# Optimization experiments

Hardware: AMD Instinct MI355X
Metric: run time of the kernel (lower is better)

## Reference

```python
import jax, jax.numpy as jnp
import numpy as np

B, C, H, W = 16, 128, 64, 64
LN_EPS = 1e-5


def _gru_dir(x, w_ih, w_hh, b_ih, b_hh, reverse):
    # x: [N, T, C]; PyTorch GRU cell math:
    # r = sig(Wir x + bir + Whr h + bhr); z = sig(Wiz x + biz + Whz h + bhz)
    xp = jnp.einsum('ntc,gc->ntg', x, w_ih) + b_ih  # [N,T,3C] precomputed input gates
    xs = jnp.swapaxes(xp, 0, 1)  # [T,N,3C]
    h0 = jnp.zeros((x.shape[0], w_hh.shape[1]), x.dtype)

    def step(h, xt):
        g = h @ w_hh.T + b_hh
        xr, xz, xn = jnp.split(xt, 3, axis=-1)
        hr, hz, hn = jnp.split(g, 3, axis=-1)
        r = jax.nn.sigmoid(xr + hr)
        z = jax.nn.sigmoid(xz + hz)
        n = jnp.tanh(xn + r * hn)
        h2 = (1.0 - z) * n + z * h
        return h2, h2

    _, ys = jax.lax.scan(step, h0, xs, reverse=reverse)
    return jnp.swapaxes(ys, 0, 1)  # [N,T,C]


def _gru_bidir(x, wih_f, whh_f, bih_f, bhh_f, wih_b, whh_b, bib_b, bhh_b):
    of = _gru_dir(x, wih_f, whh_f, bih_f, bhh_f, False)
    ob = _gru_dir(x, wih_b, whh_b, bib_b, bhh_b, True)
    return jnp.concatenate([of, ob], axis=-1)  # [N,T,2C]


def _forward(x, ln_g, ln_b,
             h_wih_f, h_whh_f, h_bih_f, h_bhh_f,
             h_wih_b, h_whh_b, h_bih_b, h_bhh_b,
             w_wih_f, w_whh_f, w_bih_f, w_bhh_f,
             w_wih_b, w_whh_b, w_bih_b, w_bhh_b,
             proj_w, proj_b):
    Bn, Cc, Hh, Ww = x.shape
    x_flat = x.reshape(Bn, Cc, Hh * Ww).transpose(0, 2, 1)  # b (h w) c
    mu = x_flat.mean(-1, keepdims=True)
    var = ((x_flat - mu) ** 2).mean(-1, keepdims=True)
    xn = (x_flat - mu) * jax.lax.rsqrt(var + LN_EPS) * ln_g + ln_b
    x4 = xn.reshape(Bn, Hh, Ww, Cc)
    # horizontal scan: rows as batch, sequence along W
    x_h = x4.reshape(Bn * Hh, Ww, Cc)
    out_h = _gru_bidir(x_h, h_wih_f, h_whh_f, h_bih_f, h_bhh_f,
                       h_wih_b, h_whh_b, h_bih_b, h_bhh_b)
    out_h = out_h.reshape(Bn, Hh * Ww, 2 * Cc)
    # vertical scan: cols as batch, sequence along H
    x_v = x4.transpose(0, 2, 1, 3).reshape(Bn * Ww, Hh, Cc)
    out_v = _gru_bidir(x_v, w_wih_f, w_whh_f, w_bih_f, w_bhh_f,
                       w_wih_b, w_whh_b, w_bih_b, w_bhh_b)
    out_v = out_v.reshape(Bn, Ww, Hh, 2 * Cc).transpose(0, 2, 1, 3).reshape(Bn, Hh * Ww, 2 * Cc)
    out = jnp.concatenate([out_h, out_v], axis=-1) @ proj_w.T + proj_b
    out = out + x_flat  # dropout in eval mode = identity
    return out.transpose(0, 2, 1).reshape(Bn, Cc, Hh, Ww)


def setup_inputs():
    key = jax.random.key(0)
    key, kx = jax.random.split(key)
    d = {
        'x': jax.random.normal(kx, (B, C, H, W), jnp.float32),
        'ln_g': jnp.ones((C,), jnp.float32),
        'ln_b': jnp.zeros((C,), jnp.float32),
    }
    bound = 1.0 / np.sqrt(C)  # torch GRU init: U(-1/sqrt(hidden), 1/sqrt(hidden))
    shapes = {'wih': (3 * C, C), 'whh': (3 * C, C), 'bih': (3 * C,), 'bhh': (3 * C,)}
    for pre in ('h', 'w'):
        for dr in ('f', 'b'):
            for p, sh in shapes.items():
                key, k1 = jax.random.split(key)
                d[f'{pre}_{p}_{dr}'] = jax.random.uniform(k1, sh, jnp.float32, -bound, bound)
    bp = 1.0 / np.sqrt(4 * C)
    key, k1, k2 = jax.random.split(key, 3)
    d['proj_w'] = jax.random.uniform(k1, (C, 4 * C), jnp.float32, -bp, bp)
    d['proj_b'] = jax.random.uniform(k2, (C,), jnp.float32, -bp, bp)
    return d


def reference(x, ln_g, ln_b,
              h_wih_f, h_whh_f, h_bih_f, h_bhh_f,
              h_wih_b, h_whh_b, h_bih_b, h_bhh_b,
              w_wih_f, w_whh_f, w_bih_f, w_bhh_f,
              w_wih_b, w_whh_b, w_bih_b, w_bhh_b,
              proj_w, proj_b):
    return _forward(x, ln_g, ln_b,
                    h_wih_f, h_whh_f, h_bih_f, h_bhh_f,
                    h_wih_b, h_whh_b, h_bih_b, h_bhh_b,
                    w_wih_f, w_whh_f, w_bih_f, w_bhh_f,
                    w_wih_b, w_whh_b, w_bih_b, w_bhh_b,
                    proj_w, proj_b)
```

## Files before the change

### kernel.cpp

```cpp
#include <hip/hip_runtime.h>

typedef short bf16x8 __attribute__((ext_vector_type(8)));
typedef float f32x4 __attribute__((ext_vector_type(4)));

static __device__ __forceinline__ unsigned short f2bf(float f) {
  unsigned u = __builtin_bit_cast(unsigned, f);
  u += 0x7FFFu + ((u >> 16) & 1u);
  return (unsigned short)(u >> 16);
}

static __device__ __forceinline__ bf16x8 pack8(const float* p) {
  float4 a = *(const float4*)p;
  float4 b = *(const float4*)(p + 4);
  bf16x8 r;
  r[0] = (short)f2bf(a.x); r[1] = (short)f2bf(a.y);
  r[2] = (short)f2bf(a.z); r[3] = (short)f2bf(a.w);
  r[4] = (short)f2bf(b.x); r[5] = (short)f2bf(b.y);
  r[6] = (short)f2bf(b.z); r[7] = (short)f2bf(b.w);
  return r;
}

__global__ __launch_bounds__(512) void pwprep_kernel(
    const float* __restrict__ pw, unsigned short* __restrict__ pwb) {
  const int i = blockIdx.x * 512 + threadIdx.x;
  pwb[i] = f2bf(pw[i]);
}

__global__ __launch_bounds__(256) void ln_kernel(
    const float* __restrict__ x, const float* __restrict__ lg,
    const float* __restrict__ lb, unsigned short* __restrict__ xn) {
  __shared__ float tile[128][65];
  __shared__ float ps[8][64];
  __shared__ float mu_s[64], rs_s[64];
  const int bid = blockIdx.x;
  const int b = bid >> 6, h = bid & 63;
  const int tid = threadIdx.x;
  const int w = tid & 63, cq = tid >> 6;
  const float* xp = x + ((size_t)(b * 128) * 64 + h) * 64 + w;
  float s1 = 0.f, s2 = 0.f;
#pragma unroll
  for (int c = cq; c < 128; c += 4) {
    float v = xp[(size_t)c * 4096];
    tile[c][w] = v;
    s1 += v; s2 += v * v;
  }
  ps[cq][w] = s1; ps[4 + cq][w] = s2;
  __syncthreads();
  if (tid < 64) {
    float a1 = ps[0][tid] + ps[1][tid] + ps[2][tid] + ps[3][tid];
    float a2 = ps[4][tid] + ps[5][tid] + ps[6][tid] + ps[7][tid];
    float mu = a1 * 0.0078125f;
    float var = a2 * 0.0078125f - mu * mu;
    mu_s[tid] = mu;
    rs_s[tid] = rsqrtf(var + 1e-5f);
  }
  __syncthreads();
  const int lane = tid & 63, w4 = tid >> 6;
  const int c0 = lane * 2;
  const float g0 = lg[c0], g1 = lg[c0 + 1], b0 = lb[c0], b1 = lb[c0 + 1];
#pragma unroll
  for (int w2 = w4; w2 < 64; w2 += 4) {
    const float mu = mu_s[w2], rs = rs_s[w2];
    float y0 = (tile[c0][w2] - mu) * rs * g0 + b0;
    float y1 = (tile[c0 + 1][w2] - mu) * rs * g1 + b1;
    unsigned pk = (unsigned)f2bf(y0) | ((unsigned)f2bf(y1) << 16);
    *(unsigned*)((unsigned char*)xn + ((size_t)((b * 64 + h) * 64 + w2)) * 256 + c0 * 2) = pk;
  }
}

__global__ __launch_bounds__(512, 2) void scan_kernel(
    const unsigned short* __restrict__ xn, unsigned short* __restrict__ cat,
    const float* __restrict__ wih0, const float* __restrict__ whh0,
    const float* __restrict__ bih0, const float* __restrict__ bhh0,
    const float* __restrict__ wih1, const float* __restrict__ whh1,
    const float* __restrict__ bih1, const float* __restrict__ bhh1,
    const float* __restrict__ wih2, const float* __restrict__ whh2,
    const float* __restrict__ bih2, const float* __restrict__ bhh2,
    const float* __restrict__ wih3, const float* __restrict__ whh3,
    const float* __restrict__ bih3, const float* __restrict__ bhh3) {
  __shared__ __align__(16) unsigned char lds[16384];
  const int tid = threadIdx.x;
  const int bid = blockIdx.x;
  const int dir = bid >> 6;
  const int grp = bid & 63;
  const int fwd = !(dir & 1);
  const int vert = dir >> 1;
  const int b = grp >> 2;
  const int r0 = (grp & 3) << 4;
  const int wv = tid >> 6;
  const int lane = tid & 63;
  const int l15 = lane & 15;
  const int l4 = lane >> 4;

  const float* wih = dir == 0 ? wih0 : dir == 1 ? wih1 : dir == 2 ? wih2 : wih3;
  const float* whh = dir == 0 ? whh0 : dir == 1 ? whh1 : dir == 2 ? whh2 : whh3;
  const float* bih = dir == 0 ? bih0 : dir == 1 ? bih1 : dir == 2 ? bih2 : bih3;
  const float* bhh = dir == 0 ? bhh0 : dir == 1 ? bhh1 : dir == 2 ? bhh2 : bhh3;

  const int ca = (wv << 4) + l15;
  bf16x8 wf[3][2][4];
#pragma unroll
  for (int g = 0; g < 3; ++g) {
#pragma unroll
    for (int s = 0; s < 2; ++s) {
      const float* Wp = s ? whh : wih;
#pragma unroll
      for (int kc = 0; kc < 4; ++kc)
        wf[g][s][kc] = pack8(Wp + (size_t)((g << 7) + ca) * 128 + (kc << 5) + (l4 << 3));
    }
  }
  const int cb = (wv << 4) + (l4 << 2);
  f32x4 br4, bz4, bnx4, bnh4;
  {
    float4 a = *(const float4*)(bih + cb), b2 = *(const float4*)(bhh + cb);
    br4[0] = a.x + b2.x; br4[1] = a.y + b2.y; br4[2] = a.z + b2.z; br4[3] = a.w + b2.w;
    a = *(const float4*)(bih + 128 + cb); b2 = *(const float4*)(bhh + 128 + cb);
    bz4[0] = a.x + b2.x; bz4[1] = a.y + b2.y; bz4[2] = a.z + b2.z; bz4[3] = a.w + b2.w;
    a = *(const float4*)(bih + 256 + cb);
    bnx4[0] = a.x; bnx4[1] = a.y; bnx4[2] = a.z; bnx4[3] = a.w;
    b2 = *(const float4*)(bhh + 256 + cb);
    bnh4[0] = b2.x; bnh4[1] = b2.y; bnh4[2] = b2.z; bnh4[3] = b2.w;
  }

  const int ss = tid >> 4, ck = tid & 15;
  const unsigned char* xsp =
      (const unsigned char*)xn +
      (vert ? ((size_t)b << 20) + (size_t)(r0 + ss) * 256 + (ck << 4)
            : ((size_t)(b * 64 + r0 + ss) << 14) + (ck << 4));
  const int xstep = vert ? 16384 : 256;
  const int sdst = (ss * 256 + (ck << 4)) ^ ((ss & 15) << 4);

  const int seq = r0 + l15;
  const int cstep = vert ? 65536 : 1024;
  unsigned char* catp =
      (unsigned char*)cat +
      ((size_t)b * 4096 + (size_t)(vert ? seq : seq * 64)) * 1024 + dir * 256 + (cb << 1) +
      (size_t)(fwd ? 0 : 63) * cstep;
  const int cdelta = fwd ? cstep : -cstep;

  *(unsigned long long*)(lds + 8192 + tid * 8) = 0ull;
  f32x4 hst = {0.f, 0.f, 0.f, 0.f};

  uint4 sX, sY;
  f32x4 grA, gzA, gnxA, grB, gzB, gnxB;
  {
    const unsigned char* xlq =
        (const unsigned char*)xn +
        (vert ? ((size_t)b << 20) + (size_t)(fwd ? 0 : 63) * 16384 + (size_t)seq * 256
              : ((size_t)(b * 64 + seq) << 14) + (size_t)(fwd ? 0 : 63) * 256) +
        (l4 << 4);
    bf16x8 x0[4];
#pragma unroll
    for (int kc = 0; kc < 4; ++kc) x0[kc] = *(const bf16x8*)(xlq + (kc << 6));
    uint4 s1v;
    if (tid < 256) {
      s1v = *(const uint4*)(xsp + (fwd ? 1 : 62) * xstep);
      sX = *(const uint4*)(xsp + (fwd ? 2 : 61) * xstep);
    }
    grA = br4; gzA = bz4; gnxA = bnx4;
#pragma unroll
    for (int kc = 0; kc < 4; ++kc) {
      grA = __builtin_amdgcn_mfma_f32_16x16x32_bf16(wf[0][0][kc], x0[kc], grA, 0, 0, 0);
      gzA = __builtin_amdgcn_mfma_f32_16x16x32_bf16(wf[1][0][kc], x0[kc], gzA, 0, 0, 0);
      gnxA = __builtin_amdgcn_mfma_f32_16x16x32_bf16(wf[2][0][kc], x0[kc], gnxA, 0, 0, 0);
    }
    if (tid < 256) *(uint4*)(lds + 4096 + sdst) = s1v;
  }
  __syncthreads();

#define STEP(TT, HCUR, HNXT, XRD, XWR, XW, XL, GRC, GZC, GNXC, GRN, GZN, GNXN)  \
  {                                                                             \
    bf16x8 ha[4], xa[4];                                                        \
    _Pragma("unroll")                                                           \
    for (int kc = 0; kc < 4; ++kc) {                                            \
      const int base = (l15 * 256 + (kc << 6) + (l4 << 4)) ^ (l15 << 4);        \
      ha[kc] = *(const bf16x8*)(lds + (HCUR) + base);                           \
      xa[kc] = *(const bf16x8*)(lds + (XRD) + base);                            \
    }                                                                           \
    if (tid < 256) {                                                            \
      *(uint4*)(lds + (XWR) + sdst) = XW;                                       \
      const int tl = (TT) + 3 > 63 ? 63 : (TT) + 3;                             \
      XL = *(const uint4*)(xsp + (fwd ? tl : 63 - tl) * xstep);                 \
    }                                                                           \
    f32x4 rh = {0.f, 0.f, 0.f, 0.f}, zh = {0.f, 0.f, 0.f, 0.f}, nh = bnh4;     \
    _Pragma("unroll")                                                           \
    for (int kc = 0; kc < 4; ++kc) {                                            \
      rh = __builtin_amdgcn_mfma_f32_16x16x32_bf16(wf[0][1][kc], ha[kc], rh, 0, 0, 0); \
      zh = __builtin_amdgcn_mfma_f32_16x16x32_bf16(wf[1][1][kc], ha[kc], zh, 0, 0, 0); \
      nh = __builtin_amdgcn_mfma_f32_16x16x32_bf16(wf[2][1][kc], ha[kc], nh, 0, 0, 0); \
    }                                                                           \
    GRN = br4; GZN = bz4; GNXN = bnx4;                                          \
    _Pragma("unroll")                                                           \
    for (int kc = 0; kc < 4; ++kc) {                                            \
      GRN = __builtin_amdgcn_mfma_f32_16x16x32_bf16(wf[0][0][kc], xa[kc], GRN, 0, 0, 0); \
      GZN = __builtin_amdgcn_mfma_f32_16x16x32_bf16(wf[1][0][kc], xa[kc], GZN, 0, 0, 0); \
      GNXN = __builtin_amdgcn_mfma_f32_16x16x32_bf16(wf[2][0][kc], xa[kc], GNXN, 0, 0, 0); \
    }                                                                           \
    f32x4 hnew;                                                                 \
    _Pragma("unroll")                                                           \
    for (int r = 0; r < 4; ++r) {                                               \
      const float rr = __builtin_amdgcn_rcpf(1.f + __expf(-(GRC[r] + rh[r]))); \
      const float zz = __builtin_amdgcn_rcpf(1.f + __expf(-(GZC[r] + zh[r]))); \
      const float pre = GNXC[r] + rr * nh[r];                                   \
      const float e2 = __expf(-2.f * pre);                                      \
      const float nn = fmaf(2.f, __builtin_amdgcn_rcpf(1.f + e2), -1.f);        \
      hnew[r] = nn + zz * (hst[r] - nn);                                        \
    }                                                                           \
    hst = hnew;                                                                 \
    unsigned hp0, hp1;                                                          \
    asm("v_cvt_pk_bf16_f32 %0, %1, %2" : "=v"(hp0) : "v"(hnew[0]), "v"(hnew[1])); \
    asm("v_cvt_pk_bf16_f32 %0, %1, %2" : "=v"(hp1) : "v"(hnew[2]), "v"(hnew[3])); \
    {                                                                           \
      unsigned long long hp = (unsigned long long)hp0 | ((unsigned long long)hp1 << 32); \
      *(unsigned long long*)(lds + (HNXT) + ((l15 * 256 + (cb << 1)) ^ (l15 << 4))) = hp; \
    }                                                                           \
    {                                                                           \
      uint2 v; v.x = hp0; v.y = hp1;                                            \
      *(uint2*)catp = v;                                                        \
      catp += cdelta;                                                           \
    }                                                                           \
    asm volatile("s_waitcnt lgkmcnt(0)" ::: "memory");                          \
    __builtin_amdgcn_s_barrier();                                               \
    asm volatile("" ::: "memory");                                              \
  }

  for (int tt2 = 0; tt2 < 64; tt2 += 2) {
    STEP(tt2, 8192, 12288, 4096, 0, sX, sY, grA, gzA, gnxA, grB, gzB, gnxB);
    STEP(tt2 + 1, 12288, 8192, 0, 4096, sY, sX, grB, gzB, gnxB, grA, gzA, gnxA);
  }
#undef STEP
}

__global__ __launch_bounds__(512, 4) void proj_kernel(
    const unsigned short* __restrict__ cat, const unsigned short* __restrict__ pwb,
    const float* __restrict__ pb, const float* __restrict__ x,
    float* __restrict__ out) {
  __shared__ __align__(16) unsigned char lds[33280];
  const int tid = threadIdx.x;
  const int bid = blockIdx.x;
  const int row0 = bid << 6;
  const int b = row0 >> 12;
  const int hw0 = row0 & 4095;
  const int wv = tid >> 6, lane = tid & 63, l15 = lane & 15, l4 = lane >> 4;

  const int cc = (wv << 4) + l15;
  bf16x8 wfr[16];
#pragma unroll
  for (int kc = 0; kc < 16; ++kc)
    wfr[kc] = *(const bf16x8*)(pwb + (size_t)cc * 512 + (kc << 5) + (l4 << 3));
  const float pbv = pb[cc];

  f32x4 acc[4];
#pragma unroll
  for (int mt = 0; mt < 4; ++mt) acc[mt] = {pbv, pbv, pbv, pbv};

#pragma unroll
  for (int s = 0; s < 2; ++s) {
#pragma unroll
    for (int it = 0; it < 4; ++it) {
      const int item = tid + (it << 9);
      const int rr = item >> 6, ckk = item & 63;
      uint4 v = *(const uint4*)((const unsigned char*)cat +
                                ((size_t)(row0 + (s << 5) + rr)) * 1024 + ckk * 16);
      *(uint4*)(lds + rr * 1024 + ((ckk ^ (rr & 7)) << 4)) = v;
    }
    __syncthreads();
#pragma unroll
    for (int mh = 0; mh < 2; ++mh) {
      const int mt = (s << 1) + mh;
      const int rl = (mh << 4) + l15;
#pragma unroll
      for (int kc = 0; kc < 16; ++kc) {
        bf16x8 af =
            *(const bf16x8*)(lds + rl * 1024 + ((((kc << 2) + l4) ^ (rl & 7)) << 4));
        acc[mt] = __builtin_amdgcn_mfma_f32_16x16x32_bf16(af, wfr[kc], acc[mt], 0, 0, 0);
      }
    }
    __syncthreads();
  }

#pragma unroll
  for (int mt = 0; mt < 4; ++mt)
#pragma unroll
    for (int j = 0; j < 4; ++j)
      *(float*)(lds + cc * 260 + (((mt << 4) + (l4 << 2) + j) << 2)) = acc[mt][j];
  __syncthreads();
#pragma unroll
  for (int it = 0; it < 16; ++it) {
    const int c = (wv << 4) + it;
    const float v = *(const float*)(lds + c * 260 + (lane << 2));
    const size_t off = (size_t)(b * 128 + c) * 4096 + hw0 + lane;
    out[off] = v + x[off];
  }
}

extern "C" void kernel_launch(void* const* d_in, const int* in_sizes, int n_in,
                              void* d_out, int out_size, void* d_ws, size_t ws_size,
                              hipStream_t stream) {
  const float* x = (const float*)d_in[0];
  const float* lg = (const float*)d_in[1];
  const float* lb = (const float*)d_in[2];
  unsigned short* xn = (unsigned short*)d_ws;
  unsigned short* cat =
      (unsigned short*)((unsigned char*)d_ws + 16777216);
  unsigned short* pwb =
      (unsigned short*)((unsigned char*)d_ws + 16777216 + 67108864);

  pwprep_kernel<<<128, 512, 0, stream>>>((const float*)d_in[19], pwb);
  ln_kernel<<<1024, 256, 0, stream>>>(x, lg, lb, xn);
  scan_kernel<<<256, 512, 0, stream>>>(
      xn, cat,
      (const float*)d_in[3], (const float*)d_in[4], (const float*)d_in[5], (const float*)d_in[6],
      (const float*)d_in[7], (const float*)d_in[8], (const float*)d_in[9], (const float*)d_in[10],
      (const float*)d_in[11], (const float*)d_in[12], (const float*)d_in[13], (const float*)d_in[14],
      (const float*)d_in[15], (const float*)d_in[16], (const float*)d_in[17], (const float*)d_in[18]);
  proj_kernel<<<1024, 512, 0, stream>>>(cat, pwb, (const float*)d_in[20], x,
                                        (float*)d_out);
}
```

Before: 126.5 us.

## Rewrite layernorm with vectorized loads and fold log2e scaling into GRU weights

The layernorm kernel is rewritten so each block handles 128 spatial positions with float4 loads across channels. Partial sums are reduced with shuffles and LDS, and results are staged through LDS so xn is written in coalesced 16-byte stores. The launch changes to 512 blocks of 512 threads. Separately, the GRU weights and biases are pre-scaled by -log2(e) or -2*log2(e) so the scan's gate nonlinearities can use the raw exp2 instruction without extra multiplies. This trims per-step VALU work on the serial critical path, at a small cost in bf16 rounding of the scaled weights.

```diff
diff --git a/kernel.cpp b/kernel.cpp
--- a/kernel.cpp
+++ b/kernel.cpp
@@ -9,16 +9,19 @@
   return (unsigned short)(u >> 16);
 }
 
-static __device__ __forceinline__ bf16x8 pack8(const float* p) {
+static __device__ __forceinline__ bf16x8 pack8s(const float* p, float s) {
   float4 a = *(const float4*)p;
   float4 b = *(const float4*)(p + 4);
   bf16x8 r;
-  r[0] = (short)f2bf(a.x); r[1] = (short)f2bf(a.y);
-  r[2] = (short)f2bf(a.z); r[3] = (short)f2bf(a.w);
-  r[4] = (short)f2bf(b.x); r[5] = (short)f2bf(b.y);
-  r[6] = (short)f2bf(b.z); r[7] = (short)f2bf(b.w);
+  r[0] = (short)f2bf(a.x * s); r[1] = (short)f2bf(a.y * s);
+  r[2] = (short)f2bf(a.z * s); r[3] = (short)f2bf(a.w * s);
+  r[4] = (short)f2bf(b.x * s); r[5] = (short)f2bf(b.y * s);
+  r[6] = (short)f2bf(b.z * s); r[7] = (short)f2bf(b.w * s);
   return r;
 }
+
+#define NLOG2E -1.442695040888963f
+#define N2LOG2E -2.885390081777927f
 
 __global__ __launch_bounds__(512) void pwprep_kernel(
     const float* __restrict__ pw, unsigned short* __restrict__ pwb) {
@@ -26,45 +29,87 @@
   pwb[i] = f2bf(pw[i]);
 }
 
-__global__ __launch_bounds__(256) void ln_kernel(
+__global__ __launch_bounds__(512, 2) void ln_kernel(
     const float* __restrict__ x, const float* __restrict__ lg,
     const float* __restrict__ lb, unsigned short* __restrict__ xn) {
-  __shared__ float tile[128][65];
-  __shared__ float ps[8][64];
-  __shared__ float mu_s[64], rs_s[64];
+  __shared__ __align__(16) unsigned char slds[35840];
+  float* mu_s = (float*)(slds + 34816);
+  float* rs_s = (float*)(slds + 35328);
+  const int tid = threadIdx.x;
   const int bid = blockIdx.x;
-  const int b = bid >> 6, h = bid & 63;
-  const int tid = threadIdx.x;
-  const int w = tid & 63, cq = tid >> 6;
-  const float* xp = x + ((size_t)(b * 128) * 64 + h) * 64 + w;
-  float s1 = 0.f, s2 = 0.f;
-#pragma unroll
-  for (int c = cq; c < 128; c += 4) {
-    float v = xp[(size_t)c * 4096];
-    tile[c][w] = v;
-    s1 += v; s2 += v * v;
-  }
-  ps[cq][w] = s1; ps[4 + cq][w] = s2;
-  __syncthreads();
-  if (tid < 64) {
-    float a1 = ps[0][tid] + ps[1][tid] + ps[2][tid] + ps[3][tid];
-    float a2 = ps[4][tid] + ps[5][tid] + ps[6][tid] + ps[7][tid];
-    float mu = a1 * 0.0078125f;
-    float var = a2 * 0.0078125f - mu * mu;
+  const int b = bid >> 5;
+  const int hw0 = (bid & 31) << 7;
+  const int q = tid >> 5, slot = tid & 31;
+  const int lane = tid & 63, wv = tid >> 6;
+
+  const float* xbase = x + ((size_t)b * 128) * 4096 + hw0 + (slot << 2);
+  float4 xv[8];
+#pragma unroll
+  for (int p = 0; p < 8; ++p)
+    xv[p] = *(const float4*)(xbase + (size_t)(q * 8 + p) * 4096);
+
+  float s1[4] = {0.f, 0.f, 0.f, 0.f}, s2[4] = {0.f, 0.f, 0.f, 0.f};
+#pragma unroll
+  for (int p = 0; p < 8; ++p) {
+    s1[0] += xv[p].x; s2[0] = fmaf(xv[p].x, xv[p].x, s2[0]);
+    s1[1] += xv[p].y; s2[1] = fmaf(xv[p].y, xv[p].y, s2[1]);
+    s1[2] += xv[p].z; s2[2] = fmaf(xv[p].z, xv[p].z, s2[2]);
+    s1[3] += xv[p].w; s2[3] = fmaf(xv[p].w, xv[p].w, s2[3]);
+  }
+#pragma unroll
+  for (int j = 0; j < 4; ++j) {
+    s1[j] += __shfl_xor(s1[j], 32);
+    s2[j] += __shfl_xor(s2[j], 32);
+  }
+  if (lane < 32) {
+    float* psp = (float*)(slds + (wv * 32 + slot) * 36);
+#pragma unroll
+    for (int j = 0; j < 4; ++j) { psp[j] = s1[j]; psp[4 + j] = s2[j]; }
+  }
+  __syncthreads();
+  if (tid < 128) {
+    const int sl2 = tid >> 2, j2 = tid & 3;
+    float a1 = 0.f, a2 = 0.f;
+#pragma unroll
+    for (int w = 0; w < 8; ++w) {
+      const float* psp = (const float*)(slds + (w * 32 + sl2) * 36);
+      a1 += psp[j2]; a2 += psp[4 + j2];
+    }
+    const float mu = a1 * 0.0078125f;
+    const float var = a2 * 0.0078125f - mu * mu;
     mu_s[tid] = mu;
     rs_s[tid] = rsqrtf(var + 1e-5f);
   }
   __syncthreads();
-  const int lane = tid & 63, w4 = tid >> 6;
-  const int c0 = lane * 2;
-  const float g0 = lg[c0], g1 = lg[c0 + 1], b0 = lb[c0], b1 = lb[c0 + 1];
-#pragma unroll
-  for (int w2 = w4; w2 < 64; w2 += 4) {
-    const float mu = mu_s[w2], rs = rs_s[w2];
-    float y0 = (tile[c0][w2] - mu) * rs * g0 + b0;
-    float y1 = (tile[c0 + 1][w2] - mu) * rs * g1 + b1;
-    unsigned pk = (unsigned)f2bf(y0) | ((unsigned)f2bf(y1) << 16);
-    *(unsigned*)((unsigned char*)xn + ((size_t)((b * 64 + h) * 64 + w2)) * 256 + c0 * 2) = pk;
+
+  float lgv[8], lbv[8];
+#pragma unroll
+  for (int p = 0; p < 8; ++p) { lgv[p] = lg[q * 8 + p]; lbv[p] = lb[q * 8 + p]; }
+#pragma unroll
+  for (int j = 0; j < 4; ++j) {
+    const int pos = (slot << 2) + j;
+    const float mu = mu_s[pos], rs = rs_s[pos];
+    float y[8];
+#pragma unroll
+    for (int p = 0; p < 8; ++p) {
+      const float xvj = j == 0 ? xv[p].x : j == 1 ? xv[p].y : j == 2 ? xv[p].z : xv[p].w;
+      y[p] = (xvj - mu) * rs * lgv[p] + lbv[p];
+    }
+    unsigned h0, h1, h2, h3;
+    asm("v_cvt_pk_bf16_f32 %0, %1, %2" : "=v"(h0) : "v"(y[0]), "v"(y[1]));
+    asm("v_cvt_pk_bf16_f32 %0, %1, %2" : "=v"(h1) : "v"(y[2]), "v"(y[3]));
+    asm("v_cvt_pk_bf16_f32 %0, %1, %2" : "=v"(h2) : "v"(y[4]), "v"(y[5]));
+    asm("v_cvt_pk_bf16_f32 %0, %1, %2" : "=v"(h3) : "v"(y[6]), "v"(y[7]));
+    uint4 v; v.x = h0; v.y = h1; v.z = h2; v.w = h3;
+    *(uint4*)(slds + pos * 272 + (q << 4)) = v;
+  }
+  __syncthreads();
+#pragma unroll
+  for (int it = 0; it < 4; ++it) {
+    const int idx = (it << 9) + tid;
+    const int row = idx >> 4, g = idx & 15;
+    uint4 v = *(const uint4*)(slds + row * 272 + (g << 4));
+    *(uint4*)((unsigned char*)xn + ((size_t)(b * 4096 + hw0 + row)) * 256 + (g << 4)) = v;
   }
 }
 
@@ -101,25 +146,30 @@
   bf16x8 wf[3][2][4];
 #pragma unroll
   for (int g = 0; g < 3; ++g) {
+    const float sc = g == 2 ? N2LOG2E : NLOG2E;
 #pragma unroll
     for (int s = 0; s < 2; ++s) {
       const float* Wp = s ? whh : wih;
 #pragma unroll
       for (int kc = 0; kc < 4; ++kc)
-        wf[g][s][kc] = pack8(Wp + (size_t)((g << 7) + ca) * 128 + (kc << 5) + (l4 << 3));
+        wf[g][s][kc] = pack8s(Wp + (size_t)((g << 7) + ca) * 128 + (kc << 5) + (l4 << 3), sc);
     }
   }
   const int cb = (wv << 4) + (l4 << 2);
   f32x4 br4, bz4, bnx4, bnh4;
   {
     float4 a = *(const float4*)(bih + cb), b2 = *(const float4*)(bhh + cb);
-    br4[0] = a.x + b2.x; br4[1] = a.y + b2.y; br4[2] = a.z + b2.z; br4[3] = a.w + b2.w;
+    br4[0] = (a.x + b2.x) * NLOG2E; br4[1] = (a.y + b2.y) * NLOG2E;
+    br4[2] = (a.z + b2.z) * NLOG2E; br4[3] = (a.w + b2.w) * NLOG2E;
     a = *(const float4*)(bih + 128 + cb); b2 = *(const float4*)(bhh + 128 + cb);
-    bz4[0] = a.x + b2.x; bz4[1] = a.y + b2.y; bz4[2] = a.z + b2.z; bz4[3] = a.w + b2.w;
+    bz4[0] = (a.x + b2.x) * NLOG2E; bz4[1] = (a.y + b2.y) * NLOG2E;
+    bz4[2] = (a.z + b2.z) * NLOG2E; bz4[3] = (a.w + b2.w) * NLOG2E;
     a = *(const float4*)(bih + 256 + cb);
-    bnx4[0] = a.x; bnx4[1] = a.y; bnx4[2] = a.z; bnx4[3] = a.w;
+    bnx4[0] = a.x * N2LOG2E; bnx4[1] = a.y * N2LOG2E;
+    bnx4[2] = a.z * N2LOG2E; bnx4[3] = a.w * N2LOG2E;
     b2 = *(const float4*)(bhh + 256 + cb);
-    bnh4[0] = b2.x; bnh4[1] = b2.y; bnh4[2] = b2.z; bnh4[3] = b2.w;
+    bnh4[0] = b2.x * N2LOG2E; bnh4[1] = b2.y * N2LOG2E;
+    bnh4[2] = b2.z * N2LOG2E; bnh4[3] = b2.w * N2LOG2E;
   }
 
   const int ss = tid >> 4, ck = tid & 15;
@@ -199,10 +249,12 @@
     f32x4 hnew;                                                                 \
     _Pragma("unroll")                                                           \
     for (int r = 0; r < 4; ++r) {                                               \
-      const float rr = __builtin_amdgcn_rcpf(1.f + __expf(-(GRC[r] + rh[r]))); \
-      const float zz = __builtin_amdgcn_rcpf(1.f + __expf(-(GZC[r] + zh[r]))); \
+      const float er = __builtin_amdgcn_exp2f(GRC[r] + rh[r]);                  \
+      const float rr = __builtin_amdgcn_rcpf(1.f + er);                         \
+      const float ez = __builtin_amdgcn_exp2f(GZC[r] + zh[r]);                  \
+      const float zz = __builtin_amdgcn_rcpf(1.f + ez);                         \
       const float pre = GNXC[r] + rr * nh[r];                                   \
-      const float e2 = __expf(-2.f * pre);                                      \
+      const float e2 = __builtin_amdgcn_exp2f(pre);                             \
       const float nn = fmaf(2.f, __builtin_amdgcn_rcpf(1.f + e2), -1.f);        \
       hnew[r] = nn + zz * (hst[r] - nn);                                        \
     }                                                                           \
@@ -307,7 +359,7 @@
       (unsigned short*)((unsigned char*)d_ws + 16777216 + 67108864);
 
   pwprep_kernel<<<128, 512, 0, stream>>>((const float*)d_in[19], pwb);
-  ln_kernel<<<1024, 256, 0, stream>>>(x, lg, lb, xn);
+  ln_kernel<<<512, 512, 0, stream>>>(x, lg, lb, xn);
   scan_kernel<<<256, 512, 0, stream>>>(
       xn, cat,
       (const float*)d_in[3], (const float*)d_in[4], (const float*)d_in[5], (const float*)d_in[6],
```

Result: faster. 118.8 us (-6.1%).
